# Performance work log

Measured on AMD Instinct MI355X. Metric: run time of the kernel, lower is better.

The kernel has to match this reference:

```python
import jax, jax.numpy as jnp
import numpy as np
from jax import lax

EPS = 1e-5  # torch BatchNorm2d default eps


def _binconv(x, w, b):
    # BinarizeConv2d: sign-binarize input and weight, dense conv, then add bias
    y = lax.conv_general_dilated(jnp.sign(x), jnp.sign(w), (2, 2), [(1, 1), (1, 1)],
                                 dimension_numbers=('NCHW', 'OIHW', 'NCHW'))
    return y + b[None, :, None, None]


def _bn(x, g, be):
    # BatchNorm2d in training mode: biased batch statistics over (N,H,W)
    m = jnp.mean(x, axis=(0, 2, 3), keepdims=True)
    v = jnp.mean((x - m) ** 2, axis=(0, 2, 3), keepdims=True)
    return (x - m) * (g[None, :, None, None] / jnp.sqrt(v + EPS)) + be[None, :, None, None]


def setup_inputs() -> dict:
    key = jax.random.key(0)
    ks = jax.random.split(key, 20)
    B = 8192
    d = {"x": jax.random.normal(ks[0], (B, 6, 32, 48), jnp.float32)}
    chans = [(12, 6), (24, 12), (48, 24), (96, 48)]
    i = 1
    for n, (co, ci) in enumerate(chans, 1):
        d[f"w{n}"] = jax.random.normal(ks[i], (co, ci, 5, 5), jnp.float32) * 0.1; i += 1
        d[f"b{n}"] = jax.random.normal(ks[i], (co,), jnp.float32) * 0.01; i += 1
        d[f"g{n}"] = jnp.ones((co,), jnp.float32)
        d[f"be{n}"] = jnp.zeros((co,), jnp.float32)
    d["wl"] = jax.random.normal(ks[i], (360, 192), jnp.float32) * 0.1; i += 1
    d["bl"] = jax.random.normal(ks[i], (360,), jnp.float32) * 0.01
    return d


def reference(x, w1, b1, g1, be1, w2, b2, g2, be2, w3, b3, g3, be3,
              w4, b4, g4, be4, wl, bl):
    x1 = jnp.clip(_bn(_binconv(x, w1, b1), g1, be1), 0.0, 1.0)
    x2 = jnp.clip(_bn(_binconv(x1, w2, b2), g2, be2), 0.0, 1.0)
    x3 = jnp.clip(_bn(_binconv(x2, w3, b3), g3, be3), 0.0, 1.0)
    x4 = jnp.clip(_bn(_binconv(x3, w4, b4), g4, be4), 0.0, 1.0)
    x4 = x4.reshape(-1, 192)  # (B, 96*1*2)
    # BinarizeLinear: in_features=192 != 784 so input is binarized too
    return jnp.sign(x4) @ jnp.sign(wl).T + bl
```

## Files before the change

### kernel.cpp

```cpp
#include <hip/hip_runtime.h>
#include <stdint.h>

typedef unsigned long long u64;
typedef uint32_t u32;
typedef uint16_t u16;

#define NIMG 8192

static const size_t O_TOT = 0;
static const size_t O_X1  = 4096;
static const size_t O_A2  = O_X1 + (size_t)NIMG*32*50*2;
static const size_t O_A3  = O_A2 + (size_t)NIMG*15*25*2;
static const size_t O_A4  = O_A3 + (size_t)NIMG*7*13*4;
static const size_t O_AL  = O_A4 + (size_t)NIMG*3*7*8;
static const size_t O_W1  = O_AL + (size_t)NIMG*3*8;
static const size_t O_W2  = O_W1 + 120*8;
static const size_t O_W3  = O_W2 + 240*8;
static const size_t O_W4  = O_W3 + 960*8;
static const size_t O_WL  = O_W4 + 3840*8;
static const size_t O_S   = O_WL + 2160*8;

__global__ void pack_w_k(const float* w1, const float* w2, const float* w3,
                         const float* w4, const float* wl,
                         u64* W1, u64* W2, u64* W3, u64* W4, u64* WL, u64* tot) {
  if (blockIdx.x == 5) {
    int t = threadIdx.x;
    tot[t] = 0; tot[t+256] = 0;
    return;
  }
  int u = blockIdx.x*256 + threadIdx.x;
  if (u < 60) {
    int co = u/5, kh = u%5;
    u64 wp=0, wn=0;
    for (int kw=0; kw<5; kw++) for (int ci=0; ci<6; ci++) {
      float v = w1[co*150 + ci*25 + kh*5 + kw];
      int pos = 6*kw + ci;
      if (v > 0.f) wp |= 1ull<<pos; else if (v < 0.f) wn |= 1ull<<pos;
    }
    W1[u*2]   = wp | (wn<<32);
    W1[u*2+1] = wn | (wp<<32);
  } else if (u < 180) {
    int t = u-60; int co=t/5, kh=t%5;
    u64 wp=0, wn=0;
    for (int kw=0; kw<5; kw++) for (int ci=0; ci<12; ci++) {
      float v = w2[co*300 + ci*25 + kh*5 + kw];
      int pos = 12*kw+ci;
      if (v>0.f) wp |= 1ull<<pos; else if (v<0.f) wn |= 1ull<<pos;
    }
    W2[t*2] = wp; W2[t*2+1] = wn;
  } else if (u < 420) {
    int t = u-180; int co=t/5, kh=t%5;
    u64 wp[2]={0,0}, wn[2]={0,0};
    for (int kw=0; kw<5; kw++) for (int ci=0; ci<24; ci++) {
      float v = w3[co*600 + ci*25 + kh*5 + kw];
      int pos = 24*kw+ci;
      if (v>0.f) wp[pos>>6] |= 1ull<<(pos&63); else if (v<0.f) wn[pos>>6] |= 1ull<<(pos&63);
    }
    W3[t*4]=wp[0]; W3[t*4+1]=wp[1]; W3[t*4+2]=wn[0]; W3[t*4+3]=wn[1];
  } else if (u < 900) {
    int t = u-420; int co=t/5, kh=t%5;
    u64 wp[4]={0,0,0,0}, wn[4]={0,0,0,0};
    for (int kw=0; kw<5; kw++) for (int ci=0; ci<48; ci++) {
      float v = w4[co*1200 + ci*25 + kh*5 + kw];
      int pos = 48*kw+ci;
      if (v>0.f) wp[pos>>6] |= 1ull<<(pos&63); else if (v<0.f) wn[pos>>6] |= 1ull<<(pos&63);
    }
    for (int j=0;j<4;j++){ W4[t*8+j]=wp[j]; W4[t*8+4+j]=wn[j]; }
  } else if (u < 1260) {
    int o = u-900;
    u64 wp[3]={0,0,0}, wn[3]={0,0,0};
    for (int k=0;k<192;k++){
      float v = wl[o*192+k];
      if (v>0.f) wp[k>>6] |= 1ull<<(k&63); else if (v<0.f) wn[k>>6] |= 1ull<<(k&63);
    }
    for (int j=0;j<3;j++){ WL[o*6+j]=wp[j]; WL[o*6+3+j]=wn[j]; }
  }
}

__global__ __launch_bounds__(256) void binx_k(const float* __restrict__ x, u16* __restrict__ X1) {
  int gid = blockIdx.x*256+threadIdx.x;
  int n = gid / 1536, r = gid % 1536, h = r/48, w = r%48;
  const float* xp = x + (size_t)n*9216 + h*48 + w;
  u32 v = 0;
  #pragma unroll
  for (int c=0;c<6;c++){ float t = xp[c*1536];
    v |= (t>0.f ? 1u:0u)<<c; v |= (t<0.f ? 1u:0u)<<(8+c); }
  u16* row = X1 + (size_t)n*1600 + h*50;
  row[w+1] = (u16)v;
  if (w==0)  row[0]  = 0;
  if (w==47) row[49] = 0;
}

__global__ __launch_bounds__(256) void conv1_k(const u16* __restrict__ X1, const u64* __restrict__ W1,
                                               u32* __restrict__ S1) {
  int pix = blockIdx.x*256+threadIdx.x;
  int n = pix/345, r = pix%345, oh = r/23, ow = r%23;
  int S[12];
  #pragma unroll
  for (int i=0;i<12;i++) S[i]=0;
  const u16* base = X1 + (size_t)n*1600;
  for (int kh=0; kh<5; kh++){
    int row = 2*oh-1+kh;
    if ((unsigned)row >= 32u) continue;
    const u16* p = base + row*50 + 2*ow;
    u64 xp=0, xn=0;
    #pragma unroll
    for (int i=0;i<5;i++){ u32 v = p[i];
      xp |= (u64)(v & 63u) << (6*i);
      xn |= (u64)(v >> 8)  << (6*i); }
    u64 X = xp | (xn<<32);
    const u64* wr = W1 + kh*2;
    #pragma unroll
    for (int co=0;co<12;co++)
      S[co] += __popcll(X & wr[co*10]) - __popcll(X & wr[co*10+1]);
  }
  u32* o = S1 + (size_t)pix*3;
  #pragma unroll
  for (int j=0;j<3;j++)
    o[j] = (u32)(S[4*j]&255) | ((u32)(S[4*j+1]&255)<<8) |
           ((u32)(S[4*j+2]&255)<<16) | ((u32)(S[4*j+3]&255)<<24);
}

__global__ __launch_bounds__(256) void conv2_k(const u16* __restrict__ A2, const u64* __restrict__ W2,
                                               short* __restrict__ S2) {
  int pix = blockIdx.x*256+threadIdx.x;
  int n = pix/77, r = pix%77, oh = r/11, ow = r%11;
  int S[24];
  #pragma unroll
  for (int i=0;i<24;i++) S[i]=0;
  const u16* base = A2 + (size_t)n*375;
  for (int kh=0; kh<5; kh++){
    int row = 2*oh-1+kh;
    if ((unsigned)row >= 15u) continue;
    const u16* p = base + row*25 + 2*ow;
    u64 X=0;
    #pragma unroll
    for (int i=0;i<5;i++) X |= (u64)p[i] << (12*i);
    const u64* wr = W2 + kh*2;
    #pragma unroll
    for (int co=0;co<24;co++)
      S[co] += __popcll(X & wr[co*10]) - __popcll(X & wr[co*10+1]);
  }
  short* o = S2 + (size_t)pix*24;
  #pragma unroll
  for (int co=0;co<24;co++) o[co] = (short)S[co];
}

__global__ __launch_bounds__(256) void conv3_k(const u32* __restrict__ A3, const u64* __restrict__ W3,
                                               short* __restrict__ S3) {
  int pix = blockIdx.x*256+threadIdx.x;
  int n = pix/15, r = pix%15, oh = r/5, ow = r%5;
  int S[48];
  #pragma unroll
  for (int i=0;i<48;i++) S[i]=0;
  const u32* base = A3 + (size_t)n*91;
  for (int kh=0; kh<5; kh++){
    int row = 2*oh-1+kh;
    if ((unsigned)row >= 7u) continue;
    const u32* p = base + row*13 + 2*ow;
    u64 a0=p[0],a1=p[1],a2=p[2],a3=p[3],a4=p[4];
    u64 x0 = a0 | (a1<<24) | (a2<<48);
    u64 x1 = (a2>>16) | (a3<<8) | (a4<<32);
    const u64* wr = W3 + kh*4;
    #pragma unroll
    for (int co=0;co<48;co++){
      const u64* q = wr + co*20;
      S[co] += __popcll(x0 & q[0]) + __popcll(x1 & q[1])
             - __popcll(x0 & q[2]) - __popcll(x1 & q[3]);
    }
  }
  short* o = S3 + (size_t)pix*48;
  #pragma unroll
  for (int co=0;co<48;co++) o[co] = (short)S[co];
}

__global__ __launch_bounds__(256) void conv4_k(const u64* __restrict__ A4, const u64* __restrict__ W4,
                                               short* __restrict__ S4) {
  int gid = blockIdx.x*256+threadIdx.x;
  int pix = gid>>2, grp = gid&3;
  int n = pix>>1, ow = pix&1;
  int S[24];
  #pragma unroll
  for (int i=0;i<24;i++) S[i]=0;
  const u64* base = A4 + (size_t)n*21;
  for (int kh=0; kh<5; kh++){
    int row = kh-1;
    if ((unsigned)row >= 3u) continue;
    const u64* p = base + row*7 + 2*ow;
    u64 a0=p[0],a1=p[1],a2=p[2],a3=p[3],a4=p[4];
    u64 x0 = a0 | (a1<<48);
    u64 x1 = (a1>>16) | (a2<<32);
    u64 x2 = (a2>>32) | (a3<<16);
    u64 x3 = a4;
    const u64* wr = W4 + kh*8;
    #pragma unroll
    for (int j=0;j<24;j++){
      const u64* q = wr + (grp*24+j)*40;
      S[j] += __popcll(x0&q[0]) + __popcll(x1&q[1]) + __popcll(x2&q[2]) + __popcll(x3&q[3])
            - __popcll(x0&q[4]) - __popcll(x1&q[5]) - __popcll(x2&q[6]) - __popcll(x3&q[7]);
    }
  }
  short* o = S4 + (size_t)pix*96 + grp*24;
  #pragma unroll
  for (int j=0;j<24;j++) o[j] = (short)S[j];
}

#define LSTR 265
template<int NR>
__device__ long long tree_reduce(const int (&vals)[NR], int* lds){
  int t = threadIdx.x;
  #pragma unroll
  for (int r=0;r<NR;r++) lds[r*LSTR + t] = vals[r];
  __syncthreads();
  if (t < NR*8) {
    int r = t % NR, seg = t / NR;
    const int* row = lds + r*LSTR + seg*32;
    int s = 0;
    #pragma unroll
    for (int i=0;i<32;i++) s += row[i];
    lds[r*LSTR + 256 + seg] = s;
  }
  __syncthreads();
  long long res = 0;
  if (t < NR) {
    const int* row = lds + t*LSTR + 256;
    int s = 0;
    #pragma unroll
    for (int i=0;i<8;i++) s += row[i];
    res = s;
  }
  __syncthreads();
  return res;
}

__global__ __launch_bounds__(256) void stats1_k(const u32* __restrict__ S1, u64* __restrict__ tot){
  __shared__ int lds[24*LSTR];
  int acc[12], q[12];
  #pragma unroll
  for (int i=0;i<12;i++){ acc[i]=0; q[i]=0; }
  int nt = gridDim.x*256;
  for (int p = blockIdx.x*256+threadIdx.x; p < NIMG*345; p += nt){
    u32 w0=S1[(size_t)p*3], w1=S1[(size_t)p*3+1], w2=S1[(size_t)p*3+2];
    #pragma unroll
    for (int c=0;c<12;c++){
      u32 w = (c<4)?w0:(c<8)?w1:w2;
      int v = (int)(w << ((3-(c&3))*8)) >> 24;
      acc[c]+=v; q[c]+=v*v;
    }
  }
  int vals[24];
  #pragma unroll
  for (int c=0;c<12;c++){ vals[c]=acc[c]; vals[12+c]=q[c]; }
  long long rs = tree_reduce<24>(vals, lds);
  int t = threadIdx.x;
  if (t < 12)       atomicAdd(&tot[t*2],        (u64)rs);
  else if (t < 24)  atomicAdd(&tot[(t-12)*2+1], (u64)rs);
}

__global__ __launch_bounds__(256) void stats2_k(const short* __restrict__ S, u64* __restrict__ tot){
  __shared__ int lds[24*LSTR];
  int acc[24], q[24];
  #pragma unroll
  for (int i=0;i<24;i++){ acc[i]=0; q[i]=0; }
  int nt = gridDim.x*256;
  for (int p = blockIdx.x*256+threadIdx.x; p < NIMG*77; p += nt){
    const int4* s4 = (const int4*)(S + (size_t)p*24);
    int4 A=s4[0], B=s4[1], Cc=s4[2];
    int w[12]={A.x,A.y,A.z,A.w,B.x,B.y,B.z,B.w,Cc.x,Cc.y,Cc.z,Cc.w};
    #pragma unroll
    for (int j=0;j<12;j++){
      int v0=(int)(short)(w[j]&0xffff), v1=w[j]>>16;
      acc[2*j]+=v0; q[2*j]+=v0*v0; acc[2*j+1]+=v1; q[2*j+1]+=v1*v1;
    }
  }
  long long rs = tree_reduce<24>(acc, lds);
  int t = threadIdx.x;
  if (t < 24) atomicAdd(&tot[t*2], (u64)rs);
  rs = tree_reduce<24>(q, lds);
  if (t < 24) atomicAdd(&tot[t*2+1], (u64)rs);
}

__global__ __launch_bounds__(256) void statsP_k(const short* __restrict__ S, u64* __restrict__ tot, int C){
  __shared__ int lds[24*LSTR];
  int pix = blockIdx.x*256+threadIdx.x;
  const short* s = S + (size_t)pix*C;
  int t = threadIdx.x;
  for (int c0=0; c0<C; c0+=24){
    const int4* s4 = (const int4*)(s + c0);
    int4 A=s4[0], B=s4[1], Cc=s4[2];
    int w[12]={A.x,A.y,A.z,A.w,B.x,B.y,B.z,B.w,Cc.x,Cc.y,Cc.z,Cc.w};
    int v[24];
    #pragma unroll
    for (int j=0;j<12;j++){ v[2*j]=(int)(short)(w[j]&0xffff); v[2*j+1]=w[j]>>16; }
    long long rs = tree_reduce<24>(v, lds);
    if (t < 24) atomicAdd(&tot[(c0+t)*2], (u64)rs);
    int vq[24];
    #pragma unroll
    for (int r=0;r<24;r++) vq[r]=v[r]*v[r];
    rs = tree_reduce<24>(vq, lds);
    if (t < 24) atomicAdd(&tot[(c0+t)*2+1], (u64)rs);
  }
}

template<int C>
__device__ void bn_params(const u64* tot, const float* g, const float* be, double cnt,
                          float* s_mu, float* s_k, float* s_be) {
  int t = threadIdx.x;
  if (t < C) {
    long long sum = (long long)tot[t*2];
    long long sq  = (long long)tot[t*2+1];
    double mu  = (double)sum / cnt;
    double var = (double)sq / cnt - mu*mu;
    double kk  = (double)g[t] / sqrt(var + 1e-5);
    s_mu[t] = (float)mu; s_k[t] = (float)kk; s_be[t] = be[t];
  }
  __syncthreads();
}

__global__ __launch_bounds__(256) void thresh1_k(const u32* __restrict__ S1, const u64* tot,
                                                 const float* g, const float* be, u16* __restrict__ A2){
  __shared__ float mu[12], kk[12], bb[12];
  bn_params<12>(tot, g, be, 2826240.0, mu, kk, bb);
  int pix = blockIdx.x*256+threadIdx.x;
  int n=pix/345, r=pix%345, oh=r/23, ow=r%23;
  const u32* s = S1 + (size_t)pix*3;
  u32 w0=s[0], w1=s[1], w2=s[2];
  u32 wv=0;
  #pragma unroll
  for (int c=0;c<12;c++){
    u32 w = (c<4) ? w0 : (c<8) ? w1 : w2;
    int sv = (int)(w << ((3-(c&3))*8)) >> 24;
    float v = ((float)sv-mu[c])*kk[c]+bb[c];
    wv |= (v>0.f?1u:0u)<<c;
  }
  u16* row = A2 + (size_t)n*375 + oh*25;
  row[ow+1] = (u16)wv;
  if (ow==0)  row[0]  = 0;
  if (ow==22) row[24] = 0;
}

__global__ __launch_bounds__(256) void thresh2_k(const short* __restrict__ S2, const u64* tot,
                                                 const float* g, const float* be, u32* __restrict__ A3){
  __shared__ float mu[24], kk[24], bb[24];
  bn_params<24>(tot, g, be, 630784.0, mu, kk, bb);
  int pix = blockIdx.x*256+threadIdx.x;
  int n=pix/77, r=pix%77, oh=r/11, ow=r%11;
  const short* s = S2 + (size_t)pix*24;
  u32 wv=0;
  #pragma unroll
  for (int c=0;c<24;c++){ float v = ((float)s[c]-mu[c])*kk[c]+bb[c]; wv |= (v>0.f?1u:0u)<<c; }
  u32* row = A3 + (size_t)n*91 + oh*13;
  row[ow+1] = wv;
  if (ow==0)  row[0]  = 0;
  if (ow==10) row[12] = 0;
}

__global__ __launch_bounds__(256) void thresh3_k(const short* __restrict__ S3, const u64* tot,
                                                 const float* g, const float* be, u64* __restrict__ A4){
  __shared__ float mu[48], kk[48], bb[48];
  bn_params<48>(tot, g, be, 122880.0, mu, kk, bb);
  int pix = blockIdx.x*256+threadIdx.x;
  int n=pix/15, r=pix%15, oh=r/5, ow=r%5;
  const short* s = S3 + (size_t)pix*48;
  u64 wv=0;
  #pragma unroll
  for (int c=0;c<48;c++){ float v = ((float)s[c]-mu[c])*kk[c]+bb[c]; wv |= (u64)(v>0.f?1u:0u)<<c; }
  u64* row = A4 + (size_t)n*21 + oh*7;
  row[ow+1] = wv;
  if (ow==0) row[0] = 0;
  if (ow==4) row[6] = 0;
}

__global__ __launch_bounds__(256) void thresh4_k(const short* __restrict__ S4, const u64* tot,
                                                 const float* g, const float* be, u64* __restrict__ aL){
  __shared__ float mu[96], kk[96], bb[96];
  bn_params<96>(tot, g, be, 16384.0, mu, kk, bb);
  int n = blockIdx.x*256+threadIdx.x;
  if (n >= NIMG) return;
  u64 a[3]={0,0,0};
  for (int w=0;w<2;w++){
    const short* s = S4 + ((size_t)n*2+w)*96;
    #pragma unroll
    for (int c=0;c<96;c++){
      float v = ((float)s[c]-mu[c])*kk[c]+bb[c];
      int k = c*2+w;
      if (v>0.f) a[k>>6] |= 1ull<<(k&63);
    }
  }
  aL[(size_t)n*3]=a[0]; aL[(size_t)n*3+1]=a[1]; aL[(size_t)n*3+2]=a[2];
}

__global__ __launch_bounds__(256) void linear_k(const u64* __restrict__ aL, const u64* __restrict__ WL,
                                                const float* __restrict__ bl, float* __restrict__ out){
  int gid = blockIdx.x*256+threadIdx.x;
  int o = gid%360, n = gid/360;
  const u64* a = aL + (size_t)n*3;
  const u64* w = WL + (size_t)o*6;
  int S = __popcll(a[0]&w[0]) + __popcll(a[1]&w[1]) + __popcll(a[2]&w[2])
        - __popcll(a[0]&w[3]) - __popcll(a[1]&w[4]) - __popcll(a[2]&w[5]);
  out[gid] = (float)S + bl[o];
}

extern "C" void kernel_launch(void* const* d_in, const int* in_sizes, int n_in,
                              void* d_out, int out_size, void* d_ws, size_t ws_size,
                              hipStream_t stream) {
  const float* x  = (const float*)d_in[0];
  const float* w1 = (const float*)d_in[1];
  const float* g1 = (const float*)d_in[3];
  const float* be1= (const float*)d_in[4];
  const float* w2 = (const float*)d_in[5];
  const float* g2 = (const float*)d_in[7];
  const float* be2= (const float*)d_in[8];
  const float* w3 = (const float*)d_in[9];
  const float* g3 = (const float*)d_in[11];
  const float* be3= (const float*)d_in[12];
  const float* w4 = (const float*)d_in[13];
  const float* g4 = (const float*)d_in[15];
  const float* be4= (const float*)d_in[16];
  const float* wl = (const float*)d_in[17];
  const float* bl = (const float*)d_in[18];

  char* ws = (char*)d_ws;
  u64* tot = (u64*)(ws + O_TOT);
  u16* X1  = (u16*)(ws + O_X1);
  u16* A2  = (u16*)(ws + O_A2);
  u32* A3  = (u32*)(ws + O_A3);
  u64* A4  = (u64*)(ws + O_A4);
  u64* aL  = (u64*)(ws + O_AL);
  u64* W1  = (u64*)(ws + O_W1);
  u64* W2  = (u64*)(ws + O_W2);
  u64* W3  = (u64*)(ws + O_W3);
  u64* W4  = (u64*)(ws + O_W4);
  u64* WL  = (u64*)(ws + O_WL);
  u32*   S1b = (u32*)(ws + O_S);
  short* Sb  = (short*)(ws + O_S);

  pack_w_k<<<6,256,0,stream>>>(w1,w2,w3,w4,wl, W1,W2,W3,W4,WL, tot);
  binx_k<<<49152,256,0,stream>>>(x, X1);

  conv1_k<<<11040,256,0,stream>>>(X1, W1, S1b);
  stats1_k<<<1024,256,0,stream>>>(S1b, tot+0);
  thresh1_k<<<11040,256,0,stream>>>(S1b, tot+0, g1, be1, A2);

  conv2_k<<<2464,256,0,stream>>>(A2, W2, Sb);
  stats2_k<<<512,256,0,stream>>>(Sb, tot+24);
  thresh2_k<<<2464,256,0,stream>>>(Sb, tot+24, g2, be2, A3);

  conv3_k<<<480,256,0,stream>>>(A3, W3, Sb);
  statsP_k<<<480,256,0,stream>>>(Sb, tot+72, 48);
  thresh3_k<<<480,256,0,stream>>>(Sb, tot+72, g3, be3, A4);

  conv4_k<<<256,256,0,stream>>>(A4, W4, Sb);
  statsP_k<<<64,256,0,stream>>>(Sb, tot+168, 96);
  thresh4_k<<<32,256,0,stream>>>(Sb, tot+168, g4, be4, aL);

  linear_k<<<11520,256,0,stream>>>(aL, WL, bl, (float*)d_out);
}
```

Before: 866.2 us.

## Fuse BN statistics into conv kernels and merge threshold with linear layer

Folds weight packing into the input binarization launch as extra blocks, and computes per-channel sum and sum-of-squares inside conv2, conv3 and conv4 through shared-memory reductions and atomics. This removes the separate stats kernels and their re-reads of the conv outputs. The layer-4 threshold and binary linear layer are merged into one kernel that keeps activations and packed weights in shared memory, which drops the aL round trip and two launches. The cost is extra syncthreads and atomics in the conv kernels, and fewer blocks for the final stage.

Result: no change. 882.2 us (+1.9%).

```diff
diff --git a/kernel.cpp b/kernel.cpp
--- a/kernel.cpp
+++ b/kernel.cpp
@@ -12,72 +12,71 @@
 static const size_t O_A2  = O_X1 + (size_t)NIMG*32*50*2;
 static const size_t O_A3  = O_A2 + (size_t)NIMG*15*25*2;
 static const size_t O_A4  = O_A3 + (size_t)NIMG*7*13*4;
-static const size_t O_AL  = O_A4 + (size_t)NIMG*3*7*8;
-static const size_t O_W1  = O_AL + (size_t)NIMG*3*8;
+static const size_t O_W1  = O_A4 + (size_t)NIMG*3*7*8;
 static const size_t O_W2  = O_W1 + 120*8;
 static const size_t O_W3  = O_W2 + 240*8;
 static const size_t O_W4  = O_W3 + 960*8;
 static const size_t O_WL  = O_W4 + 3840*8;
 static const size_t O_S   = O_WL + 2160*8;
 
-__global__ void pack_w_k(const float* w1, const float* w2, const float* w3,
+__global__ __launch_bounds__(256) void binx_k(const float* __restrict__ x,
+                         const float* w1, const float* w2, const float* w3,
                          const float* w4, const float* wl,
+                         u16* __restrict__ X1,
                          u64* W1, u64* W2, u64* W3, u64* W4, u64* WL, u64* tot) {
-  if (blockIdx.x == 5) {
+  if (blockIdx.x >= 49152) {
+    int b = blockIdx.x - 49152;
     int t = threadIdx.x;
-    tot[t] = 0; tot[t+256] = 0;
+    if (b == 5) { tot[t] = 0; tot[t+256] = 0; return; }
+    int u = b*256 + t;
+    if (u < 60) {
+      int co = u/5, kh = u%5;
+      u64 wp=0, wn=0;
+      for (int kw=0; kw<5; kw++) for (int ci=0; ci<6; ci++) {
+        float v = w1[co*150 + ci*25 + kh*5 + kw];
+        int pos = 6*kw + ci;
+        if (v > 0.f) wp |= 1ull<<pos; else if (v < 0.f) wn |= 1ull<<pos;
+      }
+      W1[u*2]   = wp | (wn<<32);
+      W1[u*2+1] = wn | (wp<<32);
+    } else if (u < 180) {
+      int q = u-60; int co=q/5, kh=q%5;
+      u64 wp=0, wn=0;
+      for (int kw=0; kw<5; kw++) for (int ci=0; ci<12; ci++) {
+        float v = w2[co*300 + ci*25 + kh*5 + kw];
+        int pos = 12*kw+ci;
+        if (v>0.f) wp |= 1ull<<pos; else if (v<0.f) wn |= 1ull<<pos;
+      }
+      W2[q*2] = wp; W2[q*2+1] = wn;
+    } else if (u < 420) {
+      int q = u-180; int co=q/5, kh=q%5;
+      u64 wp[2]={0,0}, wn[2]={0,0};
+      for (int kw=0; kw<5; kw++) for (int ci=0; ci<24; ci++) {
+        float v = w3[co*600 + ci*25 + kh*5 + kw];
+        int pos = 24*kw+ci;
+        if (v>0.f) wp[pos>>6] |= 1ull<<(pos&63); else if (v<0.f) wn[pos>>6] |= 1ull<<(pos&63);
+      }
+      W3[q*4]=wp[0]; W3[q*4+1]=wp[1]; W3[q*4+2]=wn[0]; W3[q*4+3]=wn[1];
+    } else if (u < 900) {
+      int q = u-420; int co=q/5, kh=q%5;
+      u64 wp[4]={0,0,0,0}, wn[4]={0,0,0,0};
+      for (int kw=0; kw<5; kw++) for (int ci=0; ci<48; ci++) {
+        float v = w4[co*1200 + ci*25 + kh*5 + kw];
+        int pos = 48*kw+ci;
+        if (v>0.f) wp[pos>>6] |= 1ull<<(pos&63); else if (v<0.f) wn[pos>>6] |= 1ull<<(pos&63);
+      }
+      for (int j=0;j<4;j++){ W4[q*8+j]=wp[j]; W4[q*8+4+j]=wn[j]; }
+    } else if (u < 1260) {
+      int o = u-900;
+      u64 wp[3]={0,0,0}, wn[3]={0,0,0};
+      for (int k=0;k<192;k++){
+        float v = wl[o*192+k];
+        if (v>0.f) wp[k>>6] |= 1ull<<(k&63); else if (v<0.f) wn[k>>6] |= 1ull<<(k&63);
+      }
+      for (int j=0;j<3;j++){ WL[o*6+j]=wp[j]; WL[o*6+3+j]=wn[j]; }
+    }
     return;
   }
-  int u = blockIdx.x*256 + threadIdx.x;
-  if (u < 60) {
-    int co = u/5, kh = u%5;
-    u64 wp=0, wn=0;
-    for (int kw=0; kw<5; kw++) for (int ci=0; ci<6; ci++) {
-      float v = w1[co*150 + ci*25 + kh*5 + kw];
-      int pos = 6*kw + ci;
-      if (v > 0.f) wp |= 1ull<<pos; else if (v < 0.f) wn |= 1ull<<pos;
-    }
-    W1[u*2]   = wp | (wn<<32);
-    W1[u*2+1] = wn | (wp<<32);
-  } else if (u < 180) {
-    int t = u-60; int co=t/5, kh=t%5;
-    u64 wp=0, wn=0;
-    for (int kw=0; kw<5; kw++) for (int ci=0; ci<12; ci++) {
-      float v = w2[co*300 + ci*25 + kh*5 + kw];
-      int pos = 12*kw+ci;
-      if (v>0.f) wp |= 1ull<<pos; else if (v<0.f) wn |= 1ull<<pos;
-    }
-    W2[t*2] = wp; W2[t*2+1] = wn;
-  } else if (u < 420) {
-    int t = u-180; int co=t/5, kh=t%5;
-    u64 wp[2]={0,0}, wn[2]={0,0};
-    for (int kw=0; kw<5; kw++) for (int ci=0; ci<24; ci++) {
-      float v = w3[co*600 + ci*25 + kh*5 + kw];
-      int pos = 24*kw+ci;
-      if (v>0.f) wp[pos>>6] |= 1ull<<(pos&63); else if (v<0.f) wn[pos>>6] |= 1ull<<(pos&63);
-    }
-    W3[t*4]=wp[0]; W3[t*4+1]=wp[1]; W3[t*4+2]=wn[0]; W3[t*4+3]=wn[1];
-  } else if (u < 900) {
-    int t = u-420; int co=t/5, kh=t%5;
-    u64 wp[4]={0,0,0,0}, wn[4]={0,0,0,0};
-    for (int kw=0; kw<5; kw++) for (int ci=0; ci<48; ci++) {
-      float v = w4[co*1200 + ci*25 + kh*5 + kw];
-      int pos = 48*kw+ci;
-      if (v>0.f) wp[pos>>6] |= 1ull<<(pos&63); else if (v<0.f) wn[pos>>6] |= 1ull<<(pos&63);
-    }
-    for (int j=0;j<4;j++){ W4[t*8+j]=wp[j]; W4[t*8+4+j]=wn[j]; }
-  } else if (u < 1260) {
-    int o = u-900;
-    u64 wp[3]={0,0,0}, wn[3]={0,0,0};
-    for (int k=0;k<192;k++){
-      float v = wl[o*192+k];
-      if (v>0.f) wp[k>>6] |= 1ull<<(k&63); else if (v<0.f) wn[k>>6] |= 1ull<<(k&63);
-    }
-    for (int j=0;j<3;j++){ WL[o*6+j]=wp[j]; WL[o*6+3+j]=wn[j]; }
-  }
-}
-
-__global__ __launch_bounds__(256) void binx_k(const float* __restrict__ x, u16* __restrict__ X1) {
   int gid = blockIdx.x*256+threadIdx.x;
   int n = gid / 1536, r = gid % 1536, h = r/48, w = r%48;
   const float* xp = x + (size_t)n*9216 + h*48 + w;
@@ -89,6 +88,34 @@
   row[w+1] = (u16)v;
   if (w==0)  row[0]  = 0;
   if (w==47) row[49] = 0;
+}
+
+#define LSTR 265
+template<int NR>
+__device__ long long tree_reduce(const int (&vals)[NR], int* lds){
+  int t = threadIdx.x;
+  #pragma unroll
+  for (int r=0;r<NR;r++) lds[r*LSTR + t] = vals[r];
+  __syncthreads();
+  if (t < NR*8) {
+    int r = t % NR, seg = t / NR;
+    const int* row = lds + r*LSTR + seg*32;
+    int s = 0;
+    #pragma unroll
+    for (int i=0;i<32;i++) s += row[i];
+    lds[r*LSTR + 256 + seg] = s;
+  }
+  __syncthreads();
+  long long res = 0;
+  if (t < NR) {
+    const int* row = lds + t*LSTR + 256;
+    int s = 0;
+    #pragma unroll
+    for (int i=0;i<8;i++) s += row[i];
+    res = s;
+  }
+  __syncthreads();
+  return res;
 }
 
 __global__ __launch_bounds__(256) void conv1_k(const u16* __restrict__ X1, const u64* __restrict__ W1,
@@ -121,8 +148,33 @@
            ((u32)(S[4*j+2]&255)<<16) | ((u32)(S[4*j+3]&255)<<24);
 }
 
+__global__ __launch_bounds__(256) void stats1_k(const u32* __restrict__ S1, u64* __restrict__ tot){
+  __shared__ int lds[24*LSTR];
+  int acc[12], q[12];
+  #pragma unroll
+  for (int i=0;i<12;i++){ acc[i]=0; q[i]=0; }
+  int nt = gridDim.x*256;
+  for (int p = blockIdx.x*256+threadIdx.x; p < NIMG*345; p += nt){
+    u32 w0=S1[(size_t)p*3], w1=S1[(size_t)p*3+1], w2=S1[(size_t)p*3+2];
+    #pragma unroll
+    for (int c=0;c<12;c++){
+      u32 w = (c<4)?w0:(c<8)?w1:w2;
+      int v = (int)(w << ((3-(c&3))*8)) >> 24;
+      acc[c]+=v; q[c]+=v*v;
+    }
+  }
+  int vals[24];
+  #pragma unroll
+  for (int c=0;c<12;c++){ vals[c]=acc[c]; vals[12+c]=q[c]; }
+  long long rs = tree_reduce<24>(vals, lds);
+  int t = threadIdx.x;
+  if (t < 12)       atomicAdd(&tot[t*2],        (u64)rs);
+  else if (t < 24)  atomicAdd(&tot[(t-12)*2+1], (u64)rs);
+}
+
 __global__ __launch_bounds__(256) void conv2_k(const u16* __restrict__ A2, const u64* __restrict__ W2,
-                                               short* __restrict__ S2) {
+                                               short* __restrict__ S2, u64* __restrict__ tot) {
+  __shared__ int lds[24*LSTR];
   int pix = blockIdx.x*256+threadIdx.x;
   int n = pix/77, r = pix%77, oh = r/11, ow = r%11;
   int S[24];
@@ -144,10 +196,19 @@
   short* o = S2 + (size_t)pix*24;
   #pragma unroll
   for (int co=0;co<24;co++) o[co] = (short)S[co];
+  long long rs = tree_reduce<24>(S, lds);
+  int t = threadIdx.x;
+  if (t < 24) atomicAdd(&tot[t*2], (u64)rs);
+  int q[24];
+  #pragma unroll
+  for (int c=0;c<24;c++) q[c]=S[c]*S[c];
+  rs = tree_reduce<24>(q, lds);
+  if (t < 24) atomicAdd(&tot[t*2+1], (u64)rs);
 }
 
 __global__ __launch_bounds__(256) void conv3_k(const u32* __restrict__ A3, const u64* __restrict__ W3,
-                                               short* __restrict__ S3) {
+                                               short* __restrict__ S3, u64* __restrict__ tot) {
+  __shared__ int lds[24*LSTR];
   int pix = blockIdx.x*256+threadIdx.x;
   int n = pix/15, r = pix%15, oh = r/5, ow = r%5;
   int S[48];
@@ -172,10 +233,23 @@
   short* o = S3 + (size_t)pix*48;
   #pragma unroll
   for (int co=0;co<48;co++) o[co] = (short)S[co];
+  int t = threadIdx.x;
+  for (int c0=0; c0<48; c0+=24){
+    int v[24];
+    #pragma unroll
+    for (int j=0;j<24;j++) v[j]=S[c0+j];
+    long long rs = tree_reduce<24>(v, lds);
+    if (t < 24) atomicAdd(&tot[(c0+t)*2], (u64)rs);
+    #pragma unroll
+    for (int j=0;j<24;j++) v[j]=S[c0+j]*S[c0+j];
+    rs = tree_reduce<24>(v, lds);
+    if (t < 24) atomicAdd(&tot[(c0+t)*2+1], (u64)rs);
+  }
 }
 
 __global__ __launch_bounds__(256) void conv4_k(const u64* __restrict__ A4, const u64* __restrict__ W4,
-                                               short* __restrict__ S4) {
+                                               short* __restrict__ S4, u64* __restrict__ tot) {
+  __shared__ int l4[96*66];
   int gid = blockIdx.x*256+threadIdx.x;
   int pix = gid>>2, grp = gid&3;
   int n = pix>>1, ow = pix&1;
@@ -203,102 +277,25 @@
   short* o = S4 + (size_t)pix*96 + grp*24;
   #pragma unroll
   for (int j=0;j<24;j++) o[j] = (short)S[j];
-}
-
-#define LSTR 265
-template<int NR>
-__device__ long long tree_reduce(const int (&vals)[NR], int* lds){
-  int t = threadIdx.x;
-  #pragma unroll
-  for (int r=0;r<NR;r++) lds[r*LSTR + t] = vals[r];
-  __syncthreads();
-  if (t < NR*8) {
-    int r = t % NR, seg = t / NR;
-    const int* row = lds + r*LSTR + seg*32;
-    int s = 0;
-    #pragma unroll
-    for (int i=0;i<32;i++) s += row[i];
-    lds[r*LSTR + 256 + seg] = s;
-  }
-  __syncthreads();
-  long long res = 0;
-  if (t < NR) {
-    const int* row = lds + t*LSTR + 256;
-    int s = 0;
-    #pragma unroll
-    for (int i=0;i<8;i++) s += row[i];
-    res = s;
-  }
-  __syncthreads();
-  return res;
-}
-
-__global__ __launch_bounds__(256) void stats1_k(const u32* __restrict__ S1, u64* __restrict__ tot){
-  __shared__ int lds[24*LSTR];
-  int acc[12], q[12];
-  #pragma unroll
-  for (int i=0;i<12;i++){ acc[i]=0; q[i]=0; }
-  int nt = gridDim.x*256;
-  for (int p = blockIdx.x*256+threadIdx.x; p < NIMG*345; p += nt){
-    u32 w0=S1[(size_t)p*3], w1=S1[(size_t)p*3+1], w2=S1[(size_t)p*3+2];
-    #pragma unroll
-    for (int c=0;c<12;c++){
-      u32 w = (c<4)?w0:(c<8)?w1:w2;
-      int v = (int)(w << ((3-(c&3))*8)) >> 24;
-      acc[c]+=v; q[c]+=v*v;
-    }
-  }
-  int vals[24];
-  #pragma unroll
-  for (int c=0;c<12;c++){ vals[c]=acc[c]; vals[12+c]=q[c]; }
-  long long rs = tree_reduce<24>(vals, lds);
-  int t = threadIdx.x;
-  if (t < 12)       atomicAdd(&tot[t*2],        (u64)rs);
-  else if (t < 24)  atomicAdd(&tot[(t-12)*2+1], (u64)rs);
-}
-
-__global__ __launch_bounds__(256) void stats2_k(const short* __restrict__ S, u64* __restrict__ tot){
-  __shared__ int lds[24*LSTR];
-  int acc[24], q[24];
-  #pragma unroll
-  for (int i=0;i<24;i++){ acc[i]=0; q[i]=0; }
-  int nt = gridDim.x*256;
-  for (int p = blockIdx.x*256+threadIdx.x; p < NIMG*77; p += nt){
-    const int4* s4 = (const int4*)(S + (size_t)p*24);
-    int4 A=s4[0], B=s4[1], Cc=s4[2];
-    int w[12]={A.x,A.y,A.z,A.w,B.x,B.y,B.z,B.w,Cc.x,Cc.y,Cc.z,Cc.w};
-    #pragma unroll
-    for (int j=0;j<12;j++){
-      int v0=(int)(short)(w[j]&0xffff), v1=w[j]>>16;
-      acc[2*j]+=v0; q[2*j]+=v0*v0; acc[2*j+1]+=v1; q[2*j+1]+=v1*v1;
-    }
-  }
-  long long rs = tree_reduce<24>(acc, lds);
-  int t = threadIdx.x;
-  if (t < 24) atomicAdd(&tot[t*2], (u64)rs);
-  rs = tree_reduce<24>(q, lds);
-  if (t < 24) atomicAdd(&tot[t*2+1], (u64)rs);
-}
-
-__global__ __launch_bounds__(256) void statsP_k(const short* __restrict__ S, u64* __restrict__ tot, int C){
-  __shared__ int lds[24*LSTR];
-  int pix = blockIdx.x*256+threadIdx.x;
-  const short* s = S + (size_t)pix*C;
-  int t = threadIdx.x;
-  for (int c0=0; c0<C; c0+=24){
-    const int4* s4 = (const int4*)(s + c0);
-    int4 A=s4[0], B=s4[1], Cc=s4[2];
-    int w[12]={A.x,A.y,A.z,A.w,B.x,B.y,B.z,B.w,Cc.x,Cc.y,Cc.z,Cc.w};
-    int v[24];
-    #pragma unroll
-    for (int j=0;j<12;j++){ v[2*j]=(int)(short)(w[j]&0xffff); v[2*j+1]=w[j]>>16; }
-    long long rs = tree_reduce<24>(v, lds);
-    if (t < 24) atomicAdd(&tot[(c0+t)*2], (u64)rs);
-    int vq[24];
-    #pragma unroll
-    for (int r=0;r<24;r++) vq[r]=v[r]*v[r];
-    rs = tree_reduce<24>(vq, lds);
-    if (t < 24) atomicAdd(&tot[(c0+t)*2+1], (u64)rs);
+  int t = threadIdx.x, col = t>>2;
+  #pragma unroll
+  for (int j=0;j<24;j++) l4[(grp*24+j)*66 + col] = S[j];
+  __syncthreads();
+  if (t < 96){
+    int s=0; const int* row = l4 + t*66;
+    #pragma unroll
+    for (int i=0;i<64;i++) s += row[i];
+    atomicAdd(&tot[t*2], (u64)(long long)s);
+  }
+  __syncthreads();
+  #pragma unroll
+  for (int j=0;j<24;j++) l4[(grp*24+j)*66 + col] = S[j]*S[j];
+  __syncthreads();
+  if (t < 96){
+    int s=0; const int* row = l4 + t*66;
+    #pragma unroll
+    for (int i=0;i<64;i++) s += row[i];
+    atomicAdd(&tot[t*2+1], (u64)(long long)s);
   }
 }
 
@@ -371,34 +368,42 @@
   if (ow==4) row[6] = 0;
 }
 
-__global__ __launch_bounds__(256) void thresh4_k(const short* __restrict__ S4, const u64* tot,
-                                                 const float* g, const float* be, u64* __restrict__ aL){
+__global__ __launch_bounds__(256) void lin4_k(const short* __restrict__ S4, const u64* tot,
+                                              const float* g, const float* be,
+                                              const u64* __restrict__ WL, const float* __restrict__ bl,
+                                              float* __restrict__ out){
   __shared__ float mu[96], kk[96], bb[96];
+  __shared__ u64 aLs[64*3];
+  __shared__ u64 wls[2160];
   bn_params<96>(tot, g, be, 16384.0, mu, kk, bb);
-  int n = blockIdx.x*256+threadIdx.x;
-  if (n >= NIMG) return;
-  u64 a[3]={0,0,0};
-  for (int w=0;w<2;w++){
-    const short* s = S4 + ((size_t)n*2+w)*96;
-    #pragma unroll
-    for (int c=0;c<96;c++){
-      float v = ((float)s[c]-mu[c])*kk[c]+bb[c];
-      int k = c*2+w;
-      if (v>0.f) a[k>>6] |= 1ull<<(k&63);
+  int t = threadIdx.x;
+  for (int i=t; i<2160; i+=256) wls[i] = WL[i];
+  if (t < 64){
+    int n = blockIdx.x*64 + t;
+    u64 a[3]={0,0,0};
+    for (int w=0;w<2;w++){
+      const short* s = S4 + ((size_t)n*2+w)*96;
+      #pragma unroll
+      for (int c=0;c<96;c++){
+        float v = ((float)s[c]-mu[c])*kk[c]+bb[c];
+        int k = c*2+w;
+        if (v>0.f) a[k>>6] |= 1ull<<(k&63);
+      }
     }
-  }
-  aL[(size_t)n*3]=a[0]; aL[(size_t)n*3+1]=a[1]; aL[(size_t)n*3+2]=a[2];
-}
-
-__global__ __launch_bounds__(256) void linear_k(const u64* __restrict__ aL, const u64* __restrict__ WL,
-                                                const float* __restrict__ bl, float* __restrict__ out){
-  int gid = blockIdx.x*256+threadIdx.x;
-  int o = gid%360, n = gid/360;
-  const u64* a = aL + (size_t)n*3;
-  const u64* w = WL + (size_t)o*6;
-  int S = __popcll(a[0]&w[0]) + __popcll(a[1]&w[1]) + __popcll(a[2]&w[2])
-        - __popcll(a[0]&w[3]) - __popcll(a[1]&w[4]) - __popcll(a[2]&w[5]);
-  out[gid] = (float)S + bl[o];
+    aLs[t*3]=a[0]; aLs[t*3+1]=a[1]; aLs[t*3+2]=a[2];
+  }
+  __syncthreads();
+  float* ob = out + (size_t)blockIdx.x*23040;
+  #pragma unroll 2
+  for (int i=0;i<90;i++){
+    int li = i*256+t;
+    int nl = li/360, o = li%360;
+    const u64* a = &aLs[nl*3];
+    const u64* w = &wls[o*6];
+    int S = __popcll(a[0]&w[0]) + __popcll(a[1]&w[1]) + __popcll(a[2]&w[2])
+          - __popcll(a[0]&w[3]) - __popcll(a[1]&w[4]) - __popcll(a[2]&w[5]);
+    ob[li] = (float)S + bl[o];
+  }
 }
 
 extern "C" void kernel_launch(void* const* d_in, const int* in_sizes, int n_in,
@@ -426,7 +431,6 @@
   u16* A2  = (u16*)(ws + O_A2);
   u32* A3  = (u32*)(ws + O_A3);
   u64* A4  = (u64*)(ws + O_A4);
-  u64* aL  = (u64*)(ws + O_AL);
   u64* W1  = (u64*)(ws + O_W1);
   u64* W2  = (u64*)(ws + O_W2);
   u64* W3  = (u64*)(ws + O_W3);
@@ -435,24 +439,18 @@
   u32*   S1b = (u32*)(ws + O_S);
   short* Sb  = (short*)(ws + O_S);
 
-  pack_w_k<<<6,256,0,stream>>>(w1,w2,w3,w4,wl, W1,W2,W3,W4,WL, tot);
-  binx_k<<<49152,256,0,stream>>>(x, X1);
+  binx_k<<<49158,256,0,stream>>>(x, w1,w2,w3,w4,wl, X1, W1,W2,W3,W4,WL, tot);
 
   conv1_k<<<11040,256,0,stream>>>(X1, W1, S1b);
   stats1_k<<<1024,256,0,stream>>>(S1b, tot+0);
   thresh1_k<<<11040,256,0,stream>>>(S1b, tot+0, g1, be1, A2);
 
-  conv2_k<<<2464,256,0,stream>>>(A2, W2, Sb);
-  stats2_k<<<512,256,0,stream>>>(Sb, tot+24);
+  conv2_k<<<2464,256,0,stream>>>(A2, W2, Sb, tot+24);
   thresh2_k<<<2464,256,0,stream>>>(Sb, tot+24, g2, be2, A3);
 
-  conv3_k<<<480,256,0,stream>>>(A3, W3, Sb);
-  statsP_k<<<480,256,0,stream>>>(Sb, tot+72, 48);
+  conv3_k<<<480,256,0,stream>>>(A3, W3, Sb, tot+72);
   thresh3_k<<<480,256,0,stream>>>(Sb, tot+72, g3, be3, A4);
 
-  conv4_k<<<256,256,0,stream>>>(A4, W4, Sb);
-  statsP_k<<<64,256,0,stream>>>(Sb, tot+168, 96);
-  thresh4_k<<<32,256,0,stream>>>(Sb, tot+168, g4, be4, aL);
-
-  linear_k<<<11520,256,0,stream>>>(aL, WL, bl, (float*)d_out);
-}
+  conv4_k<<<256,256,0,stream>>>(A4, W4, Sb, tot+168);
+  lin4_k<<<128,256,0,stream>>>(Sb, tot+168, g4, be4, WL, bl, (float*)d_out);
+}
```
